# Kernel tuning notes

Measured on AMD Instinct MI355X. Metric: run time of the kernel, lower is better.

## Reference

```python
import jax, jax.numpy as jnp
import numpy as np

N_NODES = 100000
N_EDGES = 600000
D_NODE = 128
D_EDGE = 128
D_HID = 512
D_OUT = 128


def setup_inputs() -> dict:
    key = jax.random.key(0)
    ks = jax.random.split(key, 8)
    node_features = jax.random.normal(ks[0], (N_NODES, D_NODE), dtype=jnp.float32)
    edge_features = jax.random.normal(ks[1], (N_EDGES, D_EDGE), dtype=jnp.float32)
    src_indices = jax.random.randint(ks[2], (N_EDGES,), 0, N_NODES, dtype=jnp.int64)
    d_in = D_NODE + D_EDGE
    W1 = jax.random.normal(ks[3], (d_in, D_HID), dtype=jnp.float32) / np.sqrt(d_in)
    b1 = jnp.zeros((D_HID,), dtype=jnp.float32)
    W2 = jax.random.normal(ks[4], (D_HID, D_OUT), dtype=jnp.float32) / np.sqrt(D_HID)
    b2 = jnp.zeros((D_OUT,), dtype=jnp.float32)
    ln_gamma = jnp.ones((D_OUT,), dtype=jnp.float32)
    ln_beta = jnp.zeros((D_OUT,), dtype=jnp.float32)
    return {
        "node_features": node_features,
        "edge_features": edge_features,
        "W1": W1, "b1": b1, "W2": W2, "b2": b2,
        "ln_gamma": ln_gamma, "ln_beta": ln_beta,
        "src_indices": src_indices,
    }


def _layer_norm(x, gamma, beta, eps=1e-5):
    mu = jnp.mean(x, axis=-1, keepdims=True)
    var = jnp.var(x, axis=-1, keepdims=True)
    return (x - mu) * jax.lax.rsqrt(var + eps) * gamma + beta


def reference(node_features, edge_features, W1, b1, W2, b2, ln_gamma, ln_beta, src_indices):
    # scatter-sum edges -> nodes  [N, D_EDGE]
    agg = jax.ops.segment_sum(edge_features, src_indices, num_segments=node_features.shape[0])
    x = jnp.concatenate([node_features, agg], axis=-1)  # [N, D_NODE+D_EDGE]
    h = jax.nn.silu(x @ W1 + b1)                         # [N, D_HID]
    y = h @ W2 + b2                                      # [N, D_OUT]
    y = _layer_norm(y, ln_gamma, ln_beta)
    return y + node_features
```

## Files before the change

### kernel.cpp

```cpp
#include <hip/hip_runtime.h>
#include <hip/hip_bf16.h>

namespace {

constexpr int N_NODES = 100000;
constexpr int N_EDGES = 600000;
constexpr int D_NODE  = 128;
constexpr int D_HID   = 512;
constexpr int D_OUT   = 128;

constexpr int CAP = 32;

constexpr int BM = 64;
constexpr int GEMM_GRID = (N_NODES + BM - 1) / BM;

typedef short bf16x8 __attribute__((ext_vector_type(8)));
typedef short bf16x4 __attribute__((ext_vector_type(4)));
typedef float f32x4  __attribute__((ext_vector_type(4)));

__device__ inline ushort f2bf(float x) {
  __hip_bfloat16 b = __float2bfloat16(x);
  return *reinterpret_cast<ushort*>(&b);
}
__device__ inline unsigned pk2(float a, float b) {
  float2 f; f.x = a; f.y = b;
  __hip_bfloat162 p = __float22bfloat162_rn(f);
  return *reinterpret_cast<unsigned*>(&p);
}

__global__ __launch_bounds__(256) void pack_w_kernel(
    const float* __restrict__ W1, const float* __restrict__ W2,
    ushort* __restrict__ W1p, ushort* __restrict__ W2p,
    int* __restrict__ cnt) {
  const int gid = blockIdx.x * 256 + threadIdx.x;
  if (gid < N_NODES) cnt[gid] = 0;
  if (gid < 16384) {
    const int l = gid & 63;
    const int kt = (gid >> 6) & 7;
    const int ntg = gid >> 9;
    const int n = ntg * 16 + (l & 15);
    const int k0 = kt * 32 + (l >> 4) * 8;
    ushort tmp[8];
#pragma unroll
    for (int j = 0; j < 8; ++j) tmp[j] = f2bf(W1[(size_t)(k0 + j) * D_HID + n]);
    *reinterpret_cast<uint4*>(W1p + (size_t)gid * 8) = *reinterpret_cast<uint4*>(tmp);
  } else if (gid < 24576) {
    const int g2 = gid - 16384;
    const int l = g2 & 63;
    const int kt = (g2 >> 6) & 15;
    const int ntg = g2 >> 10;
    const int n = ntg * 16 + (l & 15);
    const int k0 = kt * 32 + (l >> 4) * 8;
    ushort tmp[8];
#pragma unroll
    for (int j = 0; j < 8; ++j) tmp[j] = f2bf(W2[(size_t)(k0 + j) * D_OUT + n]);
    *reinterpret_cast<uint4*>(W2p + (size_t)g2 * 8) = *reinterpret_cast<uint4*>(tmp);
  }
}

__global__ __launch_bounds__(256) void bucket_fill_kernel(
    const int* __restrict__ src, int* __restrict__ cnt, int* __restrict__ elist) {
  const int e = blockIdx.x * blockDim.x + threadIdx.x;
  if (e < N_EDGES) {
    const int s = src[e];
    const int pos = atomicAdd(&cnt[s], 1);
    if (pos < CAP) elist[s * CAP + pos] = e;
  }
}


#define TR_ISSUE(kt, t0, t1)                                                        \
  {                                                                                 \
    const unsigned base_ = lds0 + (unsigned)(kt) * 1024u;                           \
    asm volatile("ds_read_b64_tr_b16 %0, %1" : "=v"(t0[0]) : "v"(base_));           \
    asm volatile("ds_read_b64_tr_b16 %0, %1 offset:512" : "=v"(t1[0]) : "v"(base_)); \
    asm volatile("ds_read_b64_tr_b16 %0, %1 offset:16384" : "=v"(t0[1]) : "v"(base_)); \
    asm volatile("ds_read_b64_tr_b16 %0, %1 offset:16896" : "=v"(t1[1]) : "v"(base_)); \
    asm volatile("ds_read_b64_tr_b16 %0, %1 offset:32768" : "=v"(t0[2]) : "v"(base_)); \
    asm volatile("ds_read_b64_tr_b16 %0, %1 offset:33280" : "=v"(t1[2]) : "v"(base_)); \
    asm volatile("ds_read_b64_tr_b16 %0, %1 offset:49152" : "=v"(t0[3]) : "v"(base_)); \
    asm volatile("ds_read_b64_tr_b16 %0, %1 offset:49664" : "=v"(t1[3]) : "v"(base_)); \
  }

#define TR_MFMA(t0, t1, bw)                                                         \
  {                                                                                 \
    _Pragma("unroll")                                                               \
    for (int mt_ = 0; mt_ < 4; ++mt_) {                                             \
      const bf16x8 am_ =                                                            \
          __builtin_shufflevector(t0[mt_], t1[mt_], 0, 1, 2, 3, 4, 5, 6, 7);        \
      acc2[mt_] = __builtin_amdgcn_mfma_f32_16x16x32_bf16(am_, bw, acc2[mt_], 0, 0, 0); \
    }                                                                               \
  }

#define LOADW2(kt)                                                                  \
  (*reinterpret_cast<const bf16x8*>(W2p + (size_t)((w * 16 + (kt)) * 64 + l) * 8))

__global__ __launch_bounds__(512, 4) void gemm_kernel(
    const float* __restrict__ nodef,
    const float* __restrict__ ef,
    const int* __restrict__ cnt,
    const int* __restrict__ elist,
    const ushort* __restrict__ W1p,
    const ushort* __restrict__ W2p,
    const float* __restrict__ b1,
    const float* __restrict__ b2,
    const float* __restrict__ gamma,
    const float* __restrict__ beta,
    float* __restrict__ out) {
  __shared__ ushort Hs[32768];
  __shared__ float mu_s[64], rs_s[64];
  float* Ys = reinterpret_cast<float*>(Hs);
  char* XsB = reinterpret_cast<char*>(Hs);

  const int t = threadIdx.x;
  const int w = t >> 6;
  const int l = t & 63;
  const int G = l >> 4;
  const int ln = l & 15;
  const int node0 = blockIdx.x * BM;

  {
    const int h = l >> 5, lc = l & 31;
#pragma unroll 1
    for (int p = 0; p < 4; ++p) {
      const int r = w * 8 + p * 2 + h;
      const int node = node0 + r;
      float4 nf = float4{0.f, 0.f, 0.f, 0.f};
      float a0 = 0.f, a1 = 0.f, a2 = 0.f, a3 = 0.f;
      int deg = 0, eidx = 0;
      if (node < N_NODES) {
        deg = min(cnt[node], CAP);
        eidx = elist[node * CAP + lc];
        nf = *reinterpret_cast<const float4*>(nodef + (size_t)node * D_NODE + 4 * lc);
      }
      int k = 0;
#pragma unroll 1
      for (; k + 4 <= deg; k += 4) {
        const int e0 = __shfl(eidx, k + 0, 32);
        const int e1 = __shfl(eidx, k + 1, 32);
        const int e2 = __shfl(eidx, k + 2, 32);
        const int e3 = __shfl(eidx, k + 3, 32);
        const float4 v0 = *reinterpret_cast<const float4*>(ef + (size_t)e0 * D_NODE + 4 * lc);
        const float4 v1 = *reinterpret_cast<const float4*>(ef + (size_t)e1 * D_NODE + 4 * lc);
        const float4 v2 = *reinterpret_cast<const float4*>(ef + (size_t)e2 * D_NODE + 4 * lc);
        const float4 v3 = *reinterpret_cast<const float4*>(ef + (size_t)e3 * D_NODE + 4 * lc);
        a0 += (v0.x + v1.x) + (v2.x + v3.x);
        a1 += (v0.y + v1.y) + (v2.y + v3.y);
        a2 += (v0.z + v1.z) + (v2.z + v3.z);
        a3 += (v0.w + v1.w) + (v2.w + v3.w);
      }
#pragma unroll 1
      for (; k < deg; ++k) {
        const int e = __shfl(eidx, k, 32);
        const float4 v = *reinterpret_cast<const float4*>(ef + (size_t)e * D_NODE + 4 * lc);
        a0 += v.x; a1 += v.y; a2 += v.z; a3 += v.w;
      }
      const unsigned sw = ((unsigned)(r & 7)) << 4;
      const unsigned rowbase = (unsigned)r * 512u;
      uint2 un; un.x = pk2(nf.x, nf.y); un.y = pk2(nf.z, nf.w);
      *reinterpret_cast<uint2*>(XsB + rowbase + (((unsigned)(lc * 8)) ^ sw)) = un;
      uint2 ua; ua.x = pk2(a0, a1); ua.y = pk2(a2, a3);
      *reinterpret_cast<uint2*>(XsB + rowbase + (((unsigned)(256 + lc * 8)) ^ sw)) = ua;
    }
  }
  __syncthreads();

  f32x4 acc[4][4];
#pragma unroll
  for (int nt = 0; nt < 4; ++nt) {
    const float bb = b1[w * 64 + nt * 16 + ln];
#pragma unroll
    for (int mt = 0; mt < 4; ++mt) acc[mt][nt] = f32x4{bb, bb, bb, bb};
  }
#pragma unroll 2
  for (int kt = 0; kt < 8; ++kt) {
    bf16x8 a[4];
#pragma unroll
    for (int mt = 0; mt < 4; ++mt) {
      const int row = mt * 16 + ln;
      const unsigned boff = (unsigned)row * 512u +
          (((unsigned)(kt * 64 + G * 16)) ^ (((unsigned)(row & 7)) << 4));
      a[mt] = *reinterpret_cast<const bf16x8*>(XsB + boff);
    }
#pragma unroll
    for (int nt = 0; nt < 4; ++nt) {
      const bf16x8 b = *reinterpret_cast<const bf16x8*>(
          W1p + (size_t)(((w * 4 + nt) * 8 + kt) * 64 + l) * 8);
#pragma unroll
      for (int mt = 0; mt < 4; ++mt)
        acc[mt][nt] = __builtin_amdgcn_mfma_f32_16x16x32_bf16(a[mt], b, acc[mt][nt], 0, 0, 0);
    }
  }
  __syncthreads();

#pragma unroll
  for (int mt = 0; mt < 4; ++mt) {
#pragma unroll
    for (int nt = 0; nt < 4; ++nt) {
      f32x4 v = acc[mt][nt];
      v.x = v.x / (1.f + __expf(-v.x));
      v.y = v.y / (1.f + __expf(-v.y));
      v.z = v.z / (1.f + __expf(-v.z));
      v.w = v.w / (1.f + __expf(-v.w));
      const int k = w * 64 + nt * 16 + ln;
      const unsigned S = (unsigned)(G * 4 + (k & 3) * 16 + ((k >> 3) & 3) * 64 +
                                    ((k >> 2) & 1) * 256 + (k >> 5) * 512 + mt * 8192);
      uint2 u;
      u.x = pk2(v.x, v.y);
      u.y = pk2(v.z, v.w);
      *reinterpret_cast<uint2*>(&Hs[S]) = u;
    }
  }
  __syncthreads();

  f32x4 acc2[4];
  {
    const float bb = b2[w * 16 + ln];
#pragma unroll
    for (int mt = 0; mt < 4; ++mt) acc2[mt] = f32x4{bb, bb, bb, bb};
  }
  const unsigned lds0 = (unsigned)(size_t)(&Hs[0]) + 8u * (unsigned)l;
  bf16x4 A0[4], A1[4], B0[4], B1[4];
  bf16x8 bwA = LOADW2(0);
  TR_ISSUE(0, A0, A1);
#pragma unroll
  for (int kp = 0; kp < 8; ++kp) {
    const int k1 = 2 * kp + 1;
    const bf16x8 bwB = LOADW2(k1);
    TR_ISSUE(k1, B0, B1);
    asm volatile("s_waitcnt lgkmcnt(8)" ::: "memory");
    __builtin_amdgcn_sched_barrier(0);
    TR_MFMA(A0, A1, bwA);
    if (kp < 7) {
      bwA = LOADW2(k1 + 1);
      TR_ISSUE(k1 + 1, A0, A1);
      asm volatile("s_waitcnt lgkmcnt(8)" ::: "memory");
    } else {
      asm volatile("s_waitcnt lgkmcnt(0)" ::: "memory");
    }
    __builtin_amdgcn_sched_barrier(0);
    TR_MFMA(B0, B1, bwB);
  }
  __syncthreads();

#pragma unroll
  for (int mt = 0; mt < 4; ++mt)
#pragma unroll
    for (int r = 0; r < 4; ++r)
      Ys[(mt * 16 + G * 4 + r) * 132 + (w * 16 + ln)] = acc2[mt][r];
  __syncthreads();
  {
    const int r = t >> 3, k2 = t & 7;
    float s = 0.f, s2 = 0.f;
#pragma unroll
    for (int u = 0; u < 16; ++u) {
      const float v = Ys[r * 132 + k2 + u * 8];
      s += v; s2 += v * v;
    }
#pragma unroll
    for (int off = 1; off < 8; off <<= 1) {
      s  += __shfl_xor(s, off);
      s2 += __shfl_xor(s2, off);
    }
    if (k2 == 0) {
      const float mu  = s * (1.f / 128.f);
      const float var = s2 * (1.f / 128.f) - mu * mu;
      mu_s[r] = mu;
      rs_s[r] = rsqrtf(var + 1e-5f);
    }
  }
  __syncthreads();
  {
    const int c = t & 127, g2 = t >> 7;
    const float gm = gamma[c], bt = beta[c];
#pragma unroll
    for (int m = 0; m < 16; ++m) {
      const int r = g2 * 16 + m;
      const int n = node0 + r;
      if (n < N_NODES) {
        out[(size_t)n * D_OUT + c] = (Ys[r * 132 + c] - mu_s[r]) * rs_s[r] * gm + bt +
                                     nodef[(size_t)n * D_NODE + c];
      }
    }
  }
}

}

extern "C" void kernel_launch(void* const* d_in, const int* in_sizes, int n_in,
                              void* d_out, int out_size, void* d_ws, size_t ws_size,
                              hipStream_t stream) {
  const float* nodef = (const float*)d_in[0];
  const float* ef    = (const float*)d_in[1];
  const float* W1    = (const float*)d_in[2];
  const float* b1    = (const float*)d_in[3];
  const float* W2    = (const float*)d_in[4];
  const float* b2    = (const float*)d_in[5];
  const float* gamma = (const float*)d_in[6];
  const float* beta  = (const float*)d_in[7];
  const int*   src   = (const int*)d_in[8];
  float* out = (float*)d_out;

  char* ws = (char*)d_ws;
  ushort* W1p   = (ushort*)ws;
  ushort* W2p   = (ushort*)(ws + 262144);
  int*    cnt   = (int*)   (ws + 393216);
  int*    elist = (int*)   (ws + 793216);

  pack_w_kernel<<<391, 256, 0, stream>>>(W1, W2, W1p, W2p, cnt);

  const int eblocks = (N_EDGES + 255) / 256;
  bucket_fill_kernel<<<eblocks, 256, 0, stream>>>(src, cnt, elist);

  gemm_kernel<<<GEMM_GRID, 512, 0, stream>>>(nodef, ef, cnt, elist, W1p, W2p,
                                             b1, b2, gamma, beta, out);
}
```

Baseline: 196.4 us.

## Halve node tile to 32 rows with 256-thread blocks and hoist gather index loads

Shrinks the fused gather+MLP+LayerNorm block from 64 to 32 nodes and from 8 to 4 waves. Each wave now covers 128 hidden columns in the first GEMM and 32 output columns in the second. Because the node count divides evenly, the row bounds checks are dropped. Degree, edge-index and node-feature loads for all four rows a wave handles are issued up front so their latency overlaps instead of serializing per row. The smaller LDS footprint and grid of twice as many blocks aim to raise occupancy and load balance for the gather-bound phase, at the cost of each block re-reading the full weight matrices for half as many rows.

```diff
diff --git a/kernel.cpp b/kernel.cpp
--- a/kernel.cpp
+++ b/kernel.cpp
@@ -11,8 +11,8 @@
 
 constexpr int CAP = 32;
 
-constexpr int BM = 64;
-constexpr int GEMM_GRID = (N_NODES + BM - 1) / BM;
+constexpr int BM = 32;
+constexpr int GEMM_GRID = N_NODES / BM;
 
 typedef short bf16x8 __attribute__((ext_vector_type(8)));
 typedef short bf16x4 __attribute__((ext_vector_type(4)));
@@ -76,26 +76,23 @@
     asm volatile("ds_read_b64_tr_b16 %0, %1 offset:512" : "=v"(t1[0]) : "v"(base_)); \
     asm volatile("ds_read_b64_tr_b16 %0, %1 offset:16384" : "=v"(t0[1]) : "v"(base_)); \
     asm volatile("ds_read_b64_tr_b16 %0, %1 offset:16896" : "=v"(t1[1]) : "v"(base_)); \
-    asm volatile("ds_read_b64_tr_b16 %0, %1 offset:32768" : "=v"(t0[2]) : "v"(base_)); \
-    asm volatile("ds_read_b64_tr_b16 %0, %1 offset:33280" : "=v"(t1[2]) : "v"(base_)); \
-    asm volatile("ds_read_b64_tr_b16 %0, %1 offset:49152" : "=v"(t0[3]) : "v"(base_)); \
-    asm volatile("ds_read_b64_tr_b16 %0, %1 offset:49664" : "=v"(t1[3]) : "v"(base_)); \
-  }
-
-#define TR_MFMA(t0, t1, bw)                                                         \
+  }
+
+#define TR_MFMA(t0, t1, bw0, bw1)                                                   \
   {                                                                                 \
     _Pragma("unroll")                                                               \
-    for (int mt_ = 0; mt_ < 4; ++mt_) {                                             \
+    for (int mt_ = 0; mt_ < 2; ++mt_) {                                             \
       const bf16x8 am_ =                                                            \
           __builtin_shufflevector(t0[mt_], t1[mt_], 0, 1, 2, 3, 4, 5, 6, 7);        \
-      acc2[mt_] = __builtin_amdgcn_mfma_f32_16x16x32_bf16(am_, bw, acc2[mt_], 0, 0, 0); \
+      acc2[mt_][0] = __builtin_amdgcn_mfma_f32_16x16x32_bf16(am_, bw0, acc2[mt_][0], 0, 0, 0); \
+      acc2[mt_][1] = __builtin_amdgcn_mfma_f32_16x16x32_bf16(am_, bw1, acc2[mt_][1], 0, 0, 0); \
     }                                                                               \
   }
 
-#define LOADW2(kt)                                                                  \
-  (*reinterpret_cast<const bf16x8*>(W2p + (size_t)((w * 16 + (kt)) * 64 + l) * 8))
-
-__global__ __launch_bounds__(512, 4) void gemm_kernel(
+#define LOADW2(nt, kt)                                                              \
+  (*reinterpret_cast<const bf16x8*>(W2p + (size_t)(((w * 2 + (nt)) * 16 + (kt)) * 64 + l) * 8))
+
+__global__ __launch_bounds__(256, 4) void gemm_kernel(
     const float* __restrict__ nodef,
     const float* __restrict__ ef,
     const int* __restrict__ cnt,
@@ -107,8 +104,8 @@
     const float* __restrict__ gamma,
     const float* __restrict__ beta,
     float* __restrict__ out) {
-  __shared__ ushort Hs[32768];
-  __shared__ float mu_s[64], rs_s[64];
+  __shared__ ushort Hs[16384];
+  __shared__ float mu_s[32], rs_s[32];
   float* Ys = reinterpret_cast<float*>(Hs);
   char* XsB = reinterpret_cast<char*>(Hs);
 
@@ -121,25 +118,27 @@
 
   {
     const int h = l >> 5, lc = l & 31;
-#pragma unroll 1
+    int deg[4]; int eidx[4]; float4 nf[4];
+#pragma unroll
     for (int p = 0; p < 4; ++p) {
       const int r = w * 8 + p * 2 + h;
       const int node = node0 + r;
-      float4 nf = float4{0.f, 0.f, 0.f, 0.f};
+      deg[p]  = min(cnt[node], CAP);
+      eidx[p] = elist[node * CAP + lc];
+      nf[p]   = *reinterpret_cast<const float4*>(nodef + (size_t)node * D_NODE + 4 * lc);
+    }
+#pragma unroll 2
+    for (int p = 0; p < 4; ++p) {
+      const int r = w * 8 + p * 2 + h;
+      const int d = deg[p];
       float a0 = 0.f, a1 = 0.f, a2 = 0.f, a3 = 0.f;
-      int deg = 0, eidx = 0;
-      if (node < N_NODES) {
-        deg = min(cnt[node], CAP);
-        eidx = elist[node * CAP + lc];
-        nf = *reinterpret_cast<const float4*>(nodef + (size_t)node * D_NODE + 4 * lc);
-      }
       int k = 0;
 #pragma unroll 1
-      for (; k + 4 <= deg; k += 4) {
-        const int e0 = __shfl(eidx, k + 0, 32);
-        const int e1 = __shfl(eidx, k + 1, 32);
-        const int e2 = __shfl(eidx, k + 2, 32);
-        const int e3 = __shfl(eidx, k + 3, 32);
+      for (; k + 4 <= d; k += 4) {
+        const int e0 = __shfl(eidx[p], k + 0, 32);
+        const int e1 = __shfl(eidx[p], k + 1, 32);
+        const int e2 = __shfl(eidx[p], k + 2, 32);
+        const int e3 = __shfl(eidx[p], k + 3, 32);
         const float4 v0 = *reinterpret_cast<const float4*>(ef + (size_t)e0 * D_NODE + 4 * lc);
         const float4 v1 = *reinterpret_cast<const float4*>(ef + (size_t)e1 * D_NODE + 4 * lc);
         const float4 v2 = *reinterpret_cast<const float4*>(ef + (size_t)e2 * D_NODE + 4 * lc);
@@ -150,14 +149,14 @@
         a3 += (v0.w + v1.w) + (v2.w + v3.w);
       }
 #pragma unroll 1
-      for (; k < deg; ++k) {
-        const int e = __shfl(eidx, k, 32);
+      for (; k < d; ++k) {
+        const int e = __shfl(eidx[p], k, 32);
         const float4 v = *reinterpret_cast<const float4*>(ef + (size_t)e * D_NODE + 4 * lc);
         a0 += v.x; a1 += v.y; a2 += v.z; a3 += v.w;
       }
       const unsigned sw = ((unsigned)(r & 7)) << 4;
       const unsigned rowbase = (unsigned)r * 512u;
-      uint2 un; un.x = pk2(nf.x, nf.y); un.y = pk2(nf.z, nf.w);
+      uint2 un; un.x = pk2(nf[p].x, nf[p].y); un.y = pk2(nf[p].z, nf[p].w);
       *reinterpret_cast<uint2*>(XsB + rowbase + (((unsigned)(lc * 8)) ^ sw)) = un;
       uint2 ua; ua.x = pk2(a0, a1); ua.y = pk2(a2, a3);
       *reinterpret_cast<uint2*>(XsB + rowbase + (((unsigned)(256 + lc * 8)) ^ sw)) = ua;
@@ -165,44 +164,44 @@
   }
   __syncthreads();
 
-  f32x4 acc[4][4];
-#pragma unroll
-  for (int nt = 0; nt < 4; ++nt) {
-    const float bb = b1[w * 64 + nt * 16 + ln];
-#pragma unroll
-    for (int mt = 0; mt < 4; ++mt) acc[mt][nt] = f32x4{bb, bb, bb, bb};
+  f32x4 acc[2][8];
+#pragma unroll
+  for (int nt = 0; nt < 8; ++nt) {
+    const float bb = b1[w * 128 + nt * 16 + ln];
+#pragma unroll
+    for (int mt = 0; mt < 2; ++mt) acc[mt][nt] = f32x4{bb, bb, bb, bb};
   }
 #pragma unroll 2
   for (int kt = 0; kt < 8; ++kt) {
-    bf16x8 a[4];
-#pragma unroll
-    for (int mt = 0; mt < 4; ++mt) {
+    bf16x8 a[2];
+#pragma unroll
+    for (int mt = 0; mt < 2; ++mt) {
       const int row = mt * 16 + ln;
       const unsigned boff = (unsigned)row * 512u +
           (((unsigned)(kt * 64 + G * 16)) ^ (((unsigned)(row & 7)) << 4));
       a[mt] = *reinterpret_cast<const bf16x8*>(XsB + boff);
     }
 #pragma unroll
-    for (int nt = 0; nt < 4; ++nt) {
+    for (int nt = 0; nt < 8; ++nt) {
       const bf16x8 b = *reinterpret_cast<const bf16x8*>(
-          W1p + (size_t)(((w * 4 + nt) * 8 + kt) * 64 + l) * 8);
-#pragma unroll
-      for (int mt = 0; mt < 4; ++mt)
+          W1p + (size_t)(((w * 8 + nt) * 8 + kt) * 64 + l) * 8);
+#pragma unroll
+      for (int mt = 0; mt < 2; ++mt)
         acc[mt][nt] = __builtin_amdgcn_mfma_f32_16x16x32_bf16(a[mt], b, acc[mt][nt], 0, 0, 0);
     }
   }
   __syncthreads();
 
 #pragma unroll
-  for (int mt = 0; mt < 4; ++mt) {
-#pragma unroll
-    for (int nt = 0; nt < 4; ++nt) {
+  for (int mt = 0; mt < 2; ++mt) {
+#pragma unroll
+    for (int nt = 0; nt < 8; ++nt) {
       f32x4 v = acc[mt][nt];
       v.x = v.x / (1.f + __expf(-v.x));
       v.y = v.y / (1.f + __expf(-v.y));
       v.z = v.z / (1.f + __expf(-v.z));
       v.w = v.w / (1.f + __expf(-v.w));
-      const int k = w * 64 + nt * 16 + ln;
+      const int k = w * 128 + nt * 16 + ln;
       const unsigned S = (unsigned)(G * 4 + (k & 3) * 16 + ((k >> 3) & 3) * 64 +
                                     ((k >> 2) & 1) * 256 + (k >> 5) * 512 + mt * 8192);
       uint2 u;
@@ -213,41 +212,46 @@
   }
   __syncthreads();
 
-  f32x4 acc2[4];
-  {
-    const float bb = b2[w * 16 + ln];
-#pragma unroll
-    for (int mt = 0; mt < 4; ++mt) acc2[mt] = f32x4{bb, bb, bb, bb};
+  f32x4 acc2[2][2];
+#pragma unroll
+  for (int nt = 0; nt < 2; ++nt) {
+    const float bb = b2[w * 32 + nt * 16 + ln];
+#pragma unroll
+    for (int mt = 0; mt < 2; ++mt) acc2[mt][nt] = f32x4{bb, bb, bb, bb};
   }
   const unsigned lds0 = (unsigned)(size_t)(&Hs[0]) + 8u * (unsigned)l;
-  bf16x4 A0[4], A1[4], B0[4], B1[4];
-  bf16x8 bwA = LOADW2(0);
+  bf16x4 A0[2], A1[2], B0[2], B1[2];
+  bf16x8 bwA0 = LOADW2(0, 0), bwA1 = LOADW2(1, 0);
   TR_ISSUE(0, A0, A1);
 #pragma unroll
   for (int kp = 0; kp < 8; ++kp) {
     const int k1 = 2 * kp + 1;
-    const bf16x8 bwB = LOADW2(k1);
+    const bf16x8 bwB0 = LOADW2(0, k1);
+    const bf16x8 bwB1 = LOADW2(1, k1);
     TR_ISSUE(k1, B0, B1);
-    asm volatile("s_waitcnt lgkmcnt(8)" ::: "memory");
+    asm volatile("s_waitcnt lgkmcnt(4)" ::: "memory");
     __builtin_amdgcn_sched_barrier(0);
-    TR_MFMA(A0, A1, bwA);
+    TR_MFMA(A0, A1, bwA0, bwA1);
     if (kp < 7) {
-      bwA = LOADW2(k1 + 1);
+      bwA0 = LOADW2(0, k1 + 1);
+      bwA1 = LOADW2(1, k1 + 1);
       TR_ISSUE(k1 + 1, A0, A1);
-      asm volatile("s_waitcnt lgkmcnt(8)" ::: "memory");
+      asm volatile("s_waitcnt lgkmcnt(4)" ::: "memory");
     } else {
       asm volatile("s_waitcnt lgkmcnt(0)" ::: "memory");
     }
     __builtin_amdgcn_sched_barrier(0);
-    TR_MFMA(B0, B1, bwB);
-  }
-  __syncthreads();
-
-#pragma unroll
-  for (int mt = 0; mt < 4; ++mt)
-#pragma unroll
-    for (int r = 0; r < 4; ++r)
-      Ys[(mt * 16 + G * 4 + r) * 132 + (w * 16 + ln)] = acc2[mt][r];
+    TR_MFMA(B0, B1, bwB0, bwB1);
+  }
+  __syncthreads();
+
+#pragma unroll
+  for (int mt = 0; mt < 2; ++mt)
+#pragma unroll
+    for (int nt = 0; nt < 2; ++nt)
+#pragma unroll
+      for (int r = 0; r < 4; ++r)
+        Ys[(mt * 16 + G * 4 + r) * 132 + (w * 32 + nt * 16 + ln)] = acc2[mt][nt][r];
   __syncthreads();
   {
     const int r = t >> 3, k2 = t & 7;
@@ -277,10 +281,8 @@
     for (int m = 0; m < 16; ++m) {
       const int r = g2 * 16 + m;
       const int n = node0 + r;
-      if (n < N_NODES) {
-        out[(size_t)n * D_OUT + c] = (Ys[r * 132 + c] - mu_s[r]) * rs_s[r] * gm + bt +
-                                     nodef[(size_t)n * D_NODE + c];
-      }
+      out[(size_t)n * D_OUT + c] = (Ys[r * 132 + c] - mu_s[r]) * rs_s[r] * gm + bt +
+                                   nodef[(size_t)n * D_NODE + c];
     }
   }
 }
@@ -312,6 +314,6 @@
   const int eblocks = (N_EDGES + 255) / 256;
   bucket_fill_kernel<<<eblocks, 256, 0, stream>>>(src, cnt, elist);
 
-  gemm_kernel<<<GEMM_GRID, 512, 0, stream>>>(nodef, ef, cnt, elist, W1p, W2p,
+  gemm_kernel<<<GEMM_GRID, 256, 0, stream>>>(nodef, ef, cnt, elist, W1p, W2p,
                                              b1, b2, gamma, beta, out);
 }
```

New measurement: 229.7 us. 1.17x slower.
